# Performance work log

Measured on AMD Instinct MI355X. Metric: run time of the kernel, lower is better.

The kernel has to match this reference:

```python
import jax, jax.numpy as jnp
import numpy as np
from jax import lax

EPS = 1e-5
GROUPS = 16


def group_norm(x, gamma, beta, g=GROUPS, eps=EPS):
    B, C, H, W = x.shape
    xr = x.reshape(B, g, C // g, H, W)
    mu = xr.mean(axis=(2, 3, 4), keepdims=True)
    var = xr.var(axis=(2, 3, 4), keepdims=True)
    xn = ((xr - mu) / jnp.sqrt(var + eps)).reshape(B, C, H, W)
    return xn * gamma[None, :, None, None] + beta[None, :, None, None]


def silu(x):
    return x * jax.nn.sigmoid(x)


def recurrence(a, b, c, d, x, axis):
    # h_t = a_t*h_{t-1} + b_t*x_t ; y_t = c_t*h_t + d_t*x_t, scanned along `axis`.
    mv = lambda t: jnp.moveaxis(t, axis, 0)
    def step(h, inp):
        at, bt, ct, dt, xt = inp
        h = at * h + bt * xt
        return h, ct * h + dt * xt
    xs = tuple(map(mv, (a, b, c, d, x)))
    h0 = jnp.zeros_like(xs[4][0])
    _, ys = lax.scan(step, h0, xs)
    return jnp.moveaxis(ys, 0, axis)


def dir_scan(x, wd, bd, axis, flip):
    # Conv1d(c,4c,1) over the scan sequence == pointwise channel linear on NCHW.
    xin = jnp.flip(x, axis) if flip else x
    coeff = jnp.einsum('oc,bchw->bohw', wd, xin) + bd[None, :, None, None]
    C = x.shape[1]
    a, b, c, d = (coeff[:, i * C:(i + 1) * C] for i in range(4))
    a = jax.nn.sigmoid(a)
    y = recurrence(a, b, c, d, xin, axis)
    return jnp.flip(y, axis) if flip else y


def setup_inputs() -> dict:
    key = jax.random.key(0)
    ks = jax.random.split(key, 10)
    B, C, H, W = 4, 128, 128, 128
    s = 1.0 / np.sqrt(C)
    inp = {
        'x': jax.random.normal(ks[0], (B, C, H, W), jnp.float32),
        'w_in': jax.random.normal(ks[1], (C, C), jnp.float32) * s,
        'gn1_gamma': jnp.ones((C,), jnp.float32),
        'gn1_beta': jnp.zeros((C,), jnp.float32),
        'w_gate': jax.random.normal(ks[2], (C, C), jnp.float32) * s,
        'b_gate': jax.random.normal(ks[3], (C,), jnp.float32) * 0.1,
        'dyn_w': jax.random.normal(ks[4], (4, 4 * C, C), jnp.float32) * s,
        'dyn_b': jax.random.normal(ks[5], (4, 4 * C), jnp.float32) * 0.1,
        'dw_kernel': jax.random.normal(ks[6], (C, 1, 3, 3), jnp.float32) * (1.0 / 3.0),
        'w_out': jax.random.normal(ks[7], (C, C), jnp.float32) * s,
        'gn2_gamma': jnp.ones((C,), jnp.float32),
        'gn2_beta': jnp.zeros((C,), jnp.float32),
    }
    return inp


def reference(x, w_in, gn1_gamma, gn1_beta, w_gate, b_gate, dyn_w, dyn_b,
              dw_kernel, w_out, gn2_gamma, gn2_beta):
    C = x.shape[1]
    # in_proj: 1x1 conv (no bias) -> GroupNorm -> SiLU
    xp = jnp.einsum('oc,bchw->bohw', w_in, x)
    xp = silu(group_norm(xp, gn1_gamma, gn1_beta))
    # 4-directional dynamic selective scans
    y_lr = dir_scan(xp, dyn_w[0], dyn_b[0], axis=3, flip=False)
    y_rl = dir_scan(xp, dyn_w[1], dyn_b[1], axis=3, flip=True)
    y_tb = dir_scan(xp, dyn_w[2], dyn_b[2], axis=2, flip=False)
    y_bt = dir_scan(xp, dyn_w[3], dyn_b[3], axis=2, flip=True)
    fused = 0.25 * (y_lr + y_rl + y_tb + y_bt)
    # gate: 1x1 conv + bias -> sigmoid, applied to projected x
    gate = jax.nn.sigmoid(jnp.einsum('oc,bchw->bohw', w_gate, xp)
                          + b_gate[None, :, None, None])
    z = fused * gate
    # out_proj: depthwise 3x3 -> 1x1 conv -> GroupNorm -> SiLU
    z = lax.conv_general_dilated(z, dw_kernel, (1, 1), ((1, 1), (1, 1)),
                                 feature_group_count=C,
                                 dimension_numbers=('NCHW', 'OIHW', 'NCHW'))
    z = jnp.einsum('oc,bchw->bohw', w_out, z)
    return silu(group_norm(z, gn2_gamma, gn2_beta))
```

## Files before the change

### kernel.cpp

```cpp
#include <hip/hip_runtime.h>
#include <math.h>

#define B_ 4
#define C_ 128
#define HW_ 16384
#define P_ 65536
#define S_ 8388608
#define CPG 8

typedef unsigned short u16;
typedef __attribute__((ext_vector_type(8))) short short8;
typedef __attribute__((ext_vector_type(4))) float f32x4;

__device__ __forceinline__ float sigmoidf_(float x){ return 1.f/(1.f+__expf(-x)); }
__device__ __forceinline__ float siluf_(float x){ return x*sigmoidf_(x); }
__device__ __forceinline__ u16 f2bf(float f){
  unsigned x = __float_as_uint(f);
  return (u16)((x + 0x7fffu + ((x >> 16) & 1u)) >> 16);
}
__device__ __forceinline__ float b2f(u16 u){ return __uint_as_float(((unsigned)u) << 16); }

__global__ __launch_bounds__(256) void prep_kernel(const float* __restrict__ dyn_w,
    const float* __restrict__ dyn_b, const float* __restrict__ w_gate,
    const float* __restrict__ w_out, const float* __restrict__ w_in,
    u16* __restrict__ wfrag, float* __restrict__ bperm, u16* __restrict__ wgbf,
    u16* __restrict__ wobf, u16* __restrict__ wibf, float* __restrict__ stats)
{
  int idx = blockIdx.x*256 + threadIdx.x;
  if (idx < 262144) {
    int e = idx & 7, lane = (idx >> 3) & 63, kk = (idx >> 9) & 3;
    int ct = (idx >> 11) & 31, d = idx >> 16;
    int m = lane & 15, kg = lane >> 4;
    int col = ct*16 + m;
    int c = col >> 2, f = col & 3;
    int k = kk*32 + kg*8 + e;
    wfrag[idx] = f2bf(dyn_w[(size_t)((d*512) + f*128 + c)*128 + k]);
  } else if (idx < 264192) {
    int i2 = idx - 262144;
    int op = i2 & 511, d = i2 >> 9;
    bperm[i2] = dyn_b[d*512 + (op & 3)*128 + (op >> 2)];
  } else if (idx < 280576) {
    wgbf[idx - 264192] = f2bf(w_gate[idx - 264192]);
  } else if (idx < 296960) {
    wobf[idx - 280576] = f2bf(w_out[idx - 280576]);
  } else if (idx < 313344) {
    wibf[idx - 296960] = f2bf(w_in[idx - 296960]);
  } else if (idx < 313600) {
    stats[idx - 313344] = 0.f;
  }
}

__global__ __launch_bounds__(256) void mfma_inproj(const float* __restrict__ x,
    const u16* __restrict__ Wm, u16* __restrict__ Out)
{
  __shared__ __align__(16) u16 st[64*136];
  int t = threadIdx.x;
  int wv = t >> 6, lane = t & 63;
  int m = lane & 15, kg = lane >> 4;
  int pt = blockIdx.x << 6;
  int b = blockIdx.x >> 8;
  int hw0 = (blockIdx.x & 255) << 6;
  const float* xb = x + ((size_t)b << 21);

  short8 Af[4][4];
  #pragma unroll
  for (int rt = 0; rt < 4; ++rt) {
    int pos = hw0 + rt*16 + m;
    #pragma unroll
    for (int kk = 0; kk < 4; ++kk) {
      short8 f;
      #pragma unroll
      for (int e = 0; e < 8; ++e)
        f[e] = (short)f2bf(xb[(size_t)(kk*32 + kg*8 + e)*HW_ + pos]);
      Af[rt][kk] = f;
    }
  }
  #pragma unroll
  for (int ct2 = 0; ct2 < 2; ++ct2) {
    int ot = wv*32 + ct2*16;
    const u16* wr = Wm + ((size_t)(ot + m) << 7) + kg*8;
    short8 Bf[4];
    #pragma unroll
    for (int kk = 0; kk < 4; ++kk)
      Bf[kk] = *(const short8*)(wr + kk*32);
    f32x4 acc[4];
    #pragma unroll
    for (int rt = 0; rt < 4; ++rt) acc[rt] = (f32x4){0.f,0.f,0.f,0.f};
    #pragma unroll
    for (int rt = 0; rt < 4; ++rt)
      #pragma unroll
      for (int kk = 0; kk < 4; ++kk)
        acc[rt] = __builtin_amdgcn_mfma_f32_16x16x32_bf16(Af[rt][kk], Bf[kk], acc[rt], 0, 0, 0);
    #pragma unroll
    for (int rt = 0; rt < 4; ++rt) {
      #pragma unroll
      for (int r = 0; r < 4; ++r)
        st[(rt*16 + kg*4 + r)*136 + ot + m] = f2bf(acc[rt][r]);
    }
  }
  __syncthreads();
  #pragma unroll
  for (int i = 0; i < 4; ++i) {
    int slot = i*256 + t;
    int row = slot >> 4, j = slot & 15;
    short8 v = *(const short8*)(st + row*136 + (j << 3));
    *(short8*)(Out + ((size_t)(pt + row) << 7) + (j << 3)) = v;
  }
}

template<int BIAS, int SIG, int GN1APPLY>
__global__ __launch_bounds__(256) void mfma_nt128(const u16* __restrict__ X,
    const u16* __restrict__ Wm, const float* __restrict__ bias, u16* __restrict__ Out,
    const float* __restrict__ stats, const float* __restrict__ gamma,
    const float* __restrict__ beta)
{
  __shared__ __align__(16) u16 st[64*136];
  int t = threadIdx.x;
  int wv = t >> 6, lane = t & 63;
  int m = lane & 15, kg = lane >> 4;
  int pt = blockIdx.x << 6;

  float ga[4][8], bb[4][8];
  if (GN1APPLY) {
    int b = blockIdx.x >> 8;
    const float cnt = (float)(CPG*HW_);
    #pragma unroll
    for (int kk = 0; kk < 4; ++kk) {
      int g = kk*4 + kg;
      float mu = stats[b*16+g]/cnt;
      float var = stats[64+b*16+g]/cnt - mu*mu;
      float rs = rsqrtf(var + 1e-5f);
      #pragma unroll
      for (int e = 0; e < 8; ++e) {
        int ch = kk*32 + kg*8 + e;
        float gm = gamma[ch] * rs;
        ga[kk][e] = gm;
        bb[kk][e] = beta[ch] - mu*gm;
      }
    }
  }

  short8 Af[4][4];
  #pragma unroll
  for (int rt = 0; rt < 4; ++rt) {
    const u16* ar = X + ((size_t)(pt + rt*16 + m) << 7) + kg*8;
    #pragma unroll
    for (int kk = 0; kk < 4; ++kk) {
      short8 v = *(const short8*)(ar + kk*32);
      if (GN1APPLY) {
        short8 o;
        #pragma unroll
        for (int e = 0; e < 8; ++e)
          o[e] = (short)f2bf(siluf_(b2f((u16)v[e])*ga[kk][e] + bb[kk][e]));
        Af[rt][kk] = o;
      } else {
        Af[rt][kk] = v;
      }
    }
  }
  #pragma unroll
  for (int ct2 = 0; ct2 < 2; ++ct2) {
    int ot = wv*32 + ct2*16;
    const u16* wr = Wm + ((size_t)(ot + m) << 7) + kg*8;
    short8 Bf[4];
    #pragma unroll
    for (int kk = 0; kk < 4; ++kk)
      Bf[kk] = *(const short8*)(wr + kk*32);
    f32x4 acc[4];
    #pragma unroll
    for (int rt = 0; rt < 4; ++rt) acc[rt] = (f32x4){0.f,0.f,0.f,0.f};
    #pragma unroll
    for (int rt = 0; rt < 4; ++rt)
      #pragma unroll
      for (int kk = 0; kk < 4; ++kk)
        acc[rt] = __builtin_amdgcn_mfma_f32_16x16x32_bf16(Af[rt][kk], Bf[kk], acc[rt], 0, 0, 0);
    float bv = BIAS ? bias[ot + m] : 0.f;
    #pragma unroll
    for (int rt = 0; rt < 4; ++rt) {
      #pragma unroll
      for (int r = 0; r < 4; ++r) {
        float v = acc[rt][r] + bv;
        if (SIG) v = sigmoidf_(v);
        st[(rt*16 + kg*4 + r)*136 + ot + m] = f2bf(v);
      }
    }
  }
  __syncthreads();
  #pragma unroll
  for (int i = 0; i < 4; ++i) {
    int slot = i*256 + t;
    int row = slot >> 4, j = slot & 15;
    short8 v = *(const short8*)(st + row*136 + (j << 3));
    *(short8*)(Out + ((size_t)(pt + row) << 7) + (j << 3)) = v;
  }
}

#define PRODUCE8(chunkv, bufv)  do { \
  int posg_ = (chunkv)*16 + m; int swp_ = (posg_ & 7) << 4; \
  short8 Bfr[4]; \
  _Pragma("unroll") for (int kk = 0; kk < 4; ++kk) \
    Bfr[kk] = *(const short8*)((char*)xs + posg_*256 + (((kk<<6)+(kg<<4)) ^ swp_)); \
  _Pragma("unroll") for (int ti = 0; ti < 8; ++ti) { \
    f32x4 acc = (f32x4){0.f,0.f,0.f,0.f}; \
    _Pragma("unroll") for (int kk = 0; kk < 4; ++kk) \
      acc = __builtin_amdgcn_mfma_f32_16x16x32_bf16(Af[ti][kk], Bfr[kk], acc, 0, 0, 0); \
    int colL_ = (tbase + ti)*16 + (kg<<2); \
    unsigned lo_ = (unsigned)f2bf(acc[0]) | ((unsigned)f2bf(acc[1])<<16); \
    unsigned hi_ = (unsigned)f2bf(acc[2]) | ((unsigned)f2bf(acc[3])<<16); \
    int byte_ = (((bufv)*2 + dw)<<14) + (m<<10) + ((colL_<<1) ^ ((m&7)<<4)); \
    *(uint2*)((char*)cs + byte_) = make_uint2(lo_, hi_); \
  } } while(0)

#define SCAN_STEP(s) { \
  float ar = b2f((u16)(cw[s].x & 0xffffu)) + bv.x; \
  float br = b2f((u16)(cw[s].x >> 16)) + bv.y; \
  float cr = b2f((u16)(cw[s].y & 0xffffu)) + bv.z; \
  float dr = b2f((u16)(cw[s].y >> 16)) + bv.w; \
  float aa = sigmoidf_(ar); \
  h = aa*h + br*xf[s]; \
  yv[s] = cr*h + dr*xf[s]; }

template<int AXISW, int PART>
__global__ __launch_bounds__(512, 2) void scan_fused(const u16* __restrict__ xpr,
    const u16* __restrict__ Wf, const float* __restrict__ bias,
    const float* __restrict__ stats, const float* __restrict__ gamma,
    const float* __restrict__ beta, u16* __restrict__ fusedP)
{
  __shared__ __align__(16) u16 xs[128*128];
  __shared__ __align__(16) u16 cs[2][2][16*512];
  __shared__ __align__(16) u16 ysL[128*128];
  int line = blockIdx.x;
  int b = line >> 7, l = line & 127;
  int t = threadIdx.x;
  int wv = t >> 6, lane = t & 63;
  int m = lane & 15, kg = lane >> 4;
  int dw = wv & 1;
  int tbase = (wv >> 1) << 3;

  {
    int cg = t & 15;
    const float cnt = (float)(CPG*HW_);
    float mu = stats[b*16+cg]/cnt;
    float var = stats[64+b*16+cg]/cnt - mu*mu;
    float rs = rsqrtf(var + 1e-5f);
    float ga[8], bb[8];
    #pragma unroll
    for (int e = 0; e < 8; ++e) {
      float gm = gamma[cg*8+e] * rs;
      ga[e] = gm;
      bb[e] = beta[cg*8+e] - mu*gm;
    }
    #pragma unroll
    for (int i = 0; i < 4; ++i) {
      int idx = i*512 + t;
      int pos = idx >> 4, j = idx & 15;
      size_t row = AXISW ? ((size_t)(b<<14) + (l<<7) + pos)
                         : ((size_t)(b<<14) + (pos<<7) + l);
      short8 v = *(const short8*)(xpr + (row<<7) + (j<<3));
      short8 o;
      #pragma unroll
      for (int e = 0; e < 8; ++e)
        o[e] = (short)f2bf(siluf_(b2f((u16)v[e])*ga[e] + bb[e]));
      int byte = pos*256 + ((j*16) ^ ((pos&7)<<4));
      *(short8*)((char*)xs + byte) = o;
    }
  }

  short8 Af[8][4];
  #pragma unroll
  for (int ti = 0; ti < 8; ++ti)
    #pragma unroll
    for (int kk = 0; kk < 4; ++kk)
      Af[ti][kk] = *(const short8*)(Wf + (size_t)(((dw*32 + tbase + ti)*4 + kk)*64 + lane)*8);

  __syncthreads();
  PRODUCE8(dw ? 7 : 0, 0);
  __syncthreads();

  int sd = (wv >> 1) & 1;
  int sc = ((wv & 1) << 6) + lane;
  float4 bv = make_float4(0.f, 0.f, 0.f, 0.f);
  if (wv < 4) bv = *(const float4*)(bias + (sd << 9) + (sc << 2));
  float h = 0.f;

  #pragma unroll 1
  for (int k = 0; k < 8; ++k) {
    if (k < 7) PRODUCE8(dw ? (6-k) : (k+1), (k+1)&1);
    if (wv < 4) {
      int chunk = sd ? (7-k) : k;
      int csb = (((k&1)*2 + sd) << 14);
      #pragma unroll
      for (int hh = 0; hh < 2; ++hh) {
        uint2 cw[8]; float xf[8];
        #pragma unroll
        for (int s = 0; s < 8; ++s) {
          int posL = sd ? (15 - (hh*8 + s)) : (hh*8 + s);
          cw[s] = *(const uint2*)((char*)cs + csb + (posL<<10) + ((sc<<3) ^ ((posL&7)<<4)));
          int pos = (chunk<<4) + posL;
          xf[s] = b2f(*(const u16*)((char*)xs + pos*256 + ((sc<<1) ^ ((posL&7)<<4))));
        }
        float yv[8];
        __builtin_amdgcn_s_setprio(1);
        #pragma unroll
        for (int s = 0; s < 8; ++s) SCAN_STEP(s)
        __builtin_amdgcn_s_setprio(0);
        #pragma unroll
        for (int s = 0; s < 8; ++s) {
          int posL = sd ? (15 - (hh*8 + s)) : (hh*8 + s);
          u16* yp = ysL + (((chunk<<4) + posL) << 7) + sc;
          if (k <= 3) *yp = f2bf(0.25f*yv[s]);
          else        *yp = f2bf(b2f(*yp) + 0.25f*yv[s]);
        }
      }
    }
    __syncthreads();
  }

  #pragma unroll
  for (int r = 0; r < 4; ++r) {
    int slot = r*512 + t;
    int pos = slot >> 4, j = slot & 15;
    short8 v = *(const short8*)(ysL + (pos << 7) + (j << 3));
    size_t rowg = AXISW ? ((size_t)(b<<14) + (l<<7) + pos)
                        : ((size_t)(b<<14) + (pos<<7) + l);
    u16* op = fusedP + (rowg << 7) + (j << 3);
    if (PART) {
      short8 o = *(const short8*)op;
      short8 rr;
      #pragma unroll
      for (int i = 0; i < 8; ++i) rr[i] = (short)f2bf(b2f((u16)v[i]) + b2f((u16)o[i]));
      *(short8*)op = rr;
    } else {
      *(short8*)op = v;
    }
  }
}

__global__ __launch_bounds__(256) void gn_stats_bf(const u16* __restrict__ X,
    float* __restrict__ stats)
{
  int b = blockIdx.x, chunk = blockIdx.y;
  const u16* base = X + ((size_t)b << 21) + ((size_t)chunk << 15);
  int t = threadIdx.x;
  float s = 0.f, q = 0.f;
  #pragma unroll 4
  for (int it = 0; it < 16; ++it) {
    short8 v = *(const short8*)(base + it*2048 + t*8);
    #pragma unroll
    for (int e = 0; e < 8; ++e) { float f = b2f((u16)v[e]); s += f; q += f*f; }
  }
  s += __shfl_xor(s, 16); q += __shfl_xor(q, 16);
  s += __shfl_xor(s, 32); q += __shfl_xor(q, 32);
  __shared__ float sg[32];
  if (t < 32) sg[t] = 0.f;
  __syncthreads();
  int lane = t & 63;
  if (lane < 16) { atomicAdd(&sg[lane], s); atomicAdd(&sg[16 + lane], q); }
  __syncthreads();
  if (t < 16) atomicAdd(&stats[b*16 + t], sg[t]);
  else if (t < 32) atomicAdd(&stats[64 + b*16 + (t - 16)], sg[t]);
}

__global__ __launch_bounds__(256) void dwconv(const u16* __restrict__ Z,
    const u16* __restrict__ G, const float* __restrict__ K9, u16* __restrict__ Outp)
{
  __shared__ float kk[1152];
  int t = threadIdx.x;
  for (int i = t; i < 1152; i += 256) kk[i] = K9[i];
  __syncthreads();
  int i4 = blockIdx.x*256 + t;
  size_t base = (size_t)i4 << 2;
  int c0 = (int)(base & 127);
  size_t p = base >> 7;
  int w = (int)(p & 127), h = (int)((p >> 7) & 127), b = (int)(p >> 14);
  float4 acc = make_float4(0.f,0.f,0.f,0.f);
  #pragma unroll
  for (int di = 0; di < 3; ++di) {
    int hy = h + di - 1;
    if ((unsigned)hy > 127u) continue;
    #pragma unroll
    for (int dj = 0; dj < 3; ++dj) {
      int wx = w + dj - 1;
      if ((unsigned)wx > 127u) continue;
      size_t p2 = ((size_t)b << 14) + (hy << 7) + wx;
      ushort4 zv = *(const ushort4*)(Z + (p2 << 7) + c0);
      ushort4 gv = *(const ushort4*)(G + (p2 << 7) + c0);
      int o = di*3 + dj;
      acc.x += b2f(zv.x) * b2f(gv.x) * kk[c0*9 + o];
      acc.y += b2f(zv.y) * b2f(gv.y) * kk[(c0+1)*9 + o];
      acc.z += b2f(zv.z) * b2f(gv.z) * kk[(c0+2)*9 + o];
      acc.w += b2f(zv.w) * b2f(gv.w) * kk[(c0+3)*9 + o];
    }
  }
  ushort4 ov;
  ov.x = f2bf(acc.x); ov.y = f2bf(acc.y); ov.z = f2bf(acc.z); ov.w = f2bf(acc.w);
  *(ushort4*)(Outp + base) = ov;
}

__global__ __launch_bounds__(256) void gn_final(const u16* __restrict__ Z,
    const float* __restrict__ stats, const float* __restrict__ gamma,
    const float* __restrict__ beta, float* __restrict__ out)
{
  __shared__ float ls[32][129];
  int w0 = blockIdx.x << 5, hh = blockIdx.y, b = blockIdx.z;
  size_t p0 = ((size_t)b << 14) + (hh << 7) + w0;
  int t = threadIdx.x;
  const float cnt = (float)(CPG*HW_);
  #pragma unroll
  for (int i = 0; i < 4; ++i) {
    int l = t + i*256;
    int row = l >> 5, c4 = (l & 31) << 2;
    ushort4 v = *(const ushort4*)(Z + ((p0 + row) << 7) + c4);
    int g = c4 >> 3;
    float mu = stats[b*16+g]/cnt;
    float var = stats[64+b*16+g]/cnt - mu*mu;
    float rs = rsqrtf(var + 1e-5f);
    float vals[4] = {b2f(v.x), b2f(v.y), b2f(v.z), b2f(v.w)};
    #pragma unroll
    for (int j = 0; j < 4; ++j) {
      float nv = (vals[j]-mu)*rs*gamma[c4+j] + beta[c4+j];
      ls[row][c4+j] = siluf_(nv);
    }
  }
  __syncthreads();
  int ww = t & 31, c0 = t >> 5;
  #pragma unroll
  for (int cc = c0; cc < 128; cc += 8) {
    out[(((size_t)(b*128 + cc)) << 14) + (hh << 7) + (w0 + ww)] = ls[ww][cc];
  }
}

extern "C" void kernel_launch(void* const* d_in, const int* in_sizes, int n_in,
                              void* d_out, int out_size, void* d_ws, size_t ws_size,
                              hipStream_t stream)
{
  (void)in_sizes; (void)n_in; (void)out_size; (void)ws_size;
  const float* x      = (const float*)d_in[0];
  const float* w_in   = (const float*)d_in[1];
  const float* g1g    = (const float*)d_in[2];
  const float* g1b    = (const float*)d_in[3];
  const float* w_gate = (const float*)d_in[4];
  const float* b_gate = (const float*)d_in[5];
  const float* dyn_w  = (const float*)d_in[6];
  const float* dyn_b  = (const float*)d_in[7];
  const float* dwk    = (const float*)d_in[8];
  const float* w_out  = (const float*)d_in[9];
  const float* g2g    = (const float*)d_in[10];
  const float* g2b    = (const float*)d_in[11];
  float* out = (float*)d_out;

  char* p = (char*)d_ws;
  u16*   Zbuf   = (u16*)p;              p += (size_t)S_*2;
  u16*   xpr    = (u16*)p;              p += (size_t)S_*2;
  u16*   fusedP = (u16*)p;              p += (size_t)S_*2;
  u16*   Gbf    = (u16*)p;              p += (size_t)S_*2;
  u16*   wfrag  = (u16*)p;              p += (size_t)262144*2;
  u16*   wgbf   = (u16*)p;              p += (size_t)16384*2;
  u16*   wobf   = (u16*)p;              p += (size_t)16384*2;
  u16*   wibf   = (u16*)p;              p += (size_t)16384*2;
  float* bperm  = (float*)p;            p += (size_t)2048*4;
  float* stats  = (float*)p;            p += (size_t)256*4;
  u16*   Zdw    = Zbuf;
  u16*   Zout   = xpr;

  prep_kernel<<<1225, 256, 0, stream>>>(dyn_w, dyn_b, w_gate, w_out, w_in,
                                        wfrag, bperm, wgbf, wobf, wibf, stats);
  mfma_inproj<<<1024, 256, 0, stream>>>(x, wibf, xpr);
  gn_stats_bf<<<dim3(4, 64), 256, 0, stream>>>(xpr, stats);

  scan_fused<1,0><<<512, 512, 0, stream>>>(xpr, wfrag, bperm, stats, g1g, g1b, fusedP);
  scan_fused<0,1><<<512, 512, 0, stream>>>(xpr, wfrag + 2*65536, bperm + 1024, stats, g1g, g1b, fusedP);

  mfma_nt128<1,1,1><<<1024, 256, 0, stream>>>(xpr, wgbf, b_gate, Gbf, stats, g1g, g1b);
  dwconv<<<8192, 256, 0, stream>>>(fusedP, Gbf, dwk, Zdw);
  mfma_nt128<0,0,0><<<1024, 256, 0, stream>>>(Zdw, wobf, nullptr, Zout, nullptr, nullptr, nullptr);
  gn_stats_bf<<<dim3(4, 64), 256, 0, stream>>>(Zout, stats + 128);
  gn_final<<<dim3(4, 128, 4), 256, 0, stream>>>(Zout, stats + 128, g2g, g2b, out);
}
```

Before: 238.0 us.

## Rebalance MFMA coefficient work away from scan warps onto idle producer warps

Warps 0-3, which run the sequential scan, now compute only 4 coefficient tiles each. Warps 4-7 compute 12 tiles each and no longer sit idle during the scan. The scan loop also handles all 16 positions of a chunk in one pass, with separate forward and reverse loop orders, instead of two half-chunks with computed index reversal. This shortens the critical path of the scan warps, but the 12-tile producer warps hold 48 short8 weight fragments, so register pressure may cause spills under the 512x2 launch bound.

New measurement: 214.3 us. -10.0%, faster.

```diff
diff --git a/kernel.cpp b/kernel.cpp
--- a/kernel.cpp
+++ b/kernel.cpp
@@ -195,12 +195,12 @@
   }
 }
 
-#define PRODUCE8(chunkv, bufv)  do { \
+#define PRODUCE(NT, bufv, chunkv)  do { \
   int posg_ = (chunkv)*16 + m; int swp_ = (posg_ & 7) << 4; \
   short8 Bfr[4]; \
   _Pragma("unroll") for (int kk = 0; kk < 4; ++kk) \
     Bfr[kk] = *(const short8*)((char*)xs + posg_*256 + (((kk<<6)+(kg<<4)) ^ swp_)); \
-  _Pragma("unroll") for (int ti = 0; ti < 8; ++ti) { \
+  _Pragma("unroll") for (int ti = 0; ti < NT; ++ti) { \
     f32x4 acc = (f32x4){0.f,0.f,0.f,0.f}; \
     _Pragma("unroll") for (int kk = 0; kk < 4; ++kk) \
       acc = __builtin_amdgcn_mfma_f32_16x16x32_bf16(Af[ti][kk], Bfr[kk], acc, 0, 0, 0); \
@@ -234,8 +234,7 @@
   int t = threadIdx.x;
   int wv = t >> 6, lane = t & 63;
   int m = lane & 15, kg = lane >> 4;
-  int dw = wv & 1;
-  int tbase = (wv >> 1) << 3;
+  int dw = (wv >> 1) & 1;
 
   {
     int cg = t & 15;
@@ -266,54 +265,77 @@
     }
   }
 
-  short8 Af[8][4];
-  #pragma unroll
-  for (int ti = 0; ti < 8; ++ti)
-    #pragma unroll
-    for (int kk = 0; kk < 4; ++kk)
-      Af[ti][kk] = *(const short8*)(Wf + (size_t)(((dw*32 + tbase + ti)*4 + kk)*64 + lane)*8);
-
-  __syncthreads();
-  PRODUCE8(dw ? 7 : 0, 0);
-  __syncthreads();
-
-  int sd = (wv >> 1) & 1;
-  int sc = ((wv & 1) << 6) + lane;
-  float4 bv = make_float4(0.f, 0.f, 0.f, 0.f);
-  if (wv < 4) bv = *(const float4*)(bias + (sd << 9) + (sc << 2));
-  float h = 0.f;
-
-  #pragma unroll 1
-  for (int k = 0; k < 8; ++k) {
-    if (k < 7) PRODUCE8(dw ? (6-k) : (k+1), (k+1)&1);
-    if (wv < 4) {
+  if (wv < 4) {
+    int tbase = (wv & 1) * 4;
+    short8 Af[4][4];
+    #pragma unroll
+    for (int ti = 0; ti < 4; ++ti)
+      #pragma unroll
+      for (int kk = 0; kk < 4; ++kk)
+        Af[ti][kk] = *(const short8*)(Wf + (size_t)(((dw*32 + tbase + ti)*4 + kk)*64 + lane)*8);
+    __syncthreads();
+    PRODUCE(4, 0, dw ? 7 : 0);
+    __syncthreads();
+
+    int sd = dw;
+    int sc = ((wv & 1) << 6) + lane;
+    float4 bv = *(const float4*)(bias + (sd << 9) + (sc << 2));
+    float h = 0.f;
+
+    #pragma unroll 1
+    for (int k = 0; k < 8; ++k) {
+      if (k < 7) PRODUCE(4, (k+1)&1, dw ? (6-k) : (k+1));
       int chunk = sd ? (7-k) : k;
       int csb = (((k&1)*2 + sd) << 14);
-      #pragma unroll
-      for (int hh = 0; hh < 2; ++hh) {
-        uint2 cw[8]; float xf[8];
+      uint2 cw[16];
+      #pragma unroll
+      for (int s = 0; s < 16; ++s)
+        cw[s] = *(const uint2*)((char*)cs + csb + (s<<10) + ((sc<<3) ^ ((s&7)<<4)));
+      float xf[16];
+      #pragma unroll
+      for (int s = 0; s < 16; ++s) {
+        int pos = (chunk<<4) + s;
+        xf[s] = b2f(*(const u16*)((char*)xs + pos*256 + ((sc<<1) ^ ((s&7)<<4))));
+      }
+      float yv[16];
+      __builtin_amdgcn_s_setprio(1);
+      if (sd == 0) {
         #pragma unroll
-        for (int s = 0; s < 8; ++s) {
-          int posL = sd ? (15 - (hh*8 + s)) : (hh*8 + s);
-          cw[s] = *(const uint2*)((char*)cs + csb + (posL<<10) + ((sc<<3) ^ ((posL&7)<<4)));
-          int pos = (chunk<<4) + posL;
-          xf[s] = b2f(*(const u16*)((char*)xs + pos*256 + ((sc<<1) ^ ((posL&7)<<4))));
-        }
-        float yv[8];
-        __builtin_amdgcn_s_setprio(1);
+        for (int s = 0; s < 16; ++s) SCAN_STEP(s)
+      } else {
         #pragma unroll
-        for (int s = 0; s < 8; ++s) SCAN_STEP(s)
-        __builtin_amdgcn_s_setprio(0);
+        for (int s = 15; s >= 0; --s) SCAN_STEP(s)
+      }
+      __builtin_amdgcn_s_setprio(0);
+      u16* yrow = ysL + (chunk << 11) + sc;
+      if (k <= 3) {
         #pragma unroll
-        for (int s = 0; s < 8; ++s) {
-          int posL = sd ? (15 - (hh*8 + s)) : (hh*8 + s);
-          u16* yp = ysL + (((chunk<<4) + posL) << 7) + sc;
-          if (k <= 3) *yp = f2bf(0.25f*yv[s]);
-          else        *yp = f2bf(b2f(*yp) + 0.25f*yv[s]);
+        for (int s = 0; s < 16; ++s) yrow[s << 7] = f2bf(0.25f*yv[s]);
+      } else {
+        #pragma unroll
+        for (int s = 0; s < 16; ++s) {
+          float o = b2f(yrow[s << 7]);
+          yrow[s << 7] = f2bf(o + 0.25f*yv[s]);
         }
       }
-    }
+      __syncthreads();
+    }
+  } else {
+    int tbase = 8 + (wv & 1) * 12;
+    short8 Af[12][4];
+    #pragma unroll
+    for (int ti = 0; ti < 12; ++ti)
+      #pragma unroll
+      for (int kk = 0; kk < 4; ++kk)
+        Af[ti][kk] = *(const short8*)(Wf + (size_t)(((dw*32 + tbase + ti)*4 + kk)*64 + lane)*8);
     __syncthreads();
+    PRODUCE(12, 0, dw ? 7 : 0);
+    __syncthreads();
+    #pragma unroll 1
+    for (int k = 0; k < 8; ++k) {
+      if (k < 7) PRODUCE(12, (k+1)&1, dw ? (6-k) : (k+1));
+      __syncthreads();
+    }
   }
 
   #pragma unroll
```
